# Optimization experiments

Measured on AMD Instinct MI355X. Metric: run time of the kernel, lower is better.

## Reference

```python
import jax, jax.numpy as jnp
import numpy as np

B, L, D, H = 4, 1024, 1024, 16
HD = D // H            # head_dim = 64
MAX_LEN = 1024         # pos_max_len
SCALE = HD ** 0.5


def setup_inputs() -> dict:
    key = jax.random.key(0)
    ks = jax.random.split(key, 7)
    sd = 1.0 / np.sqrt(D)
    x = jax.random.normal(ks[0], (B, L, D), dtype=jnp.float32)
    Wq = jax.random.normal(ks[1], (D, D), dtype=jnp.float32) * sd
    Wk = jax.random.normal(ks[2], (D, D), dtype=jnp.float32) * sd
    Wv = jax.random.normal(ks[3], (D, D), dtype=jnp.float32) * sd
    Wo = jax.random.normal(ks[4], (D, D), dtype=jnp.float32) * sd
    # relative positional embedding tables [2*max_len+1, head_dim]
    pek = jax.random.normal(ks[5], (2 * MAX_LEN + 1, HD), dtype=jnp.float32) / np.sqrt(HD)
    pev = jax.random.normal(ks[6], (2 * MAX_LEN + 1, HD), dtype=jnp.float32) / np.sqrt(HD)
    return {"x": x, "Wq": Wq, "Wk": Wk, "Wv": Wv, "Wo": Wo, "pek": pek, "pev": pev}


def _rel_idx(seq_len):
    r = jnp.arange(seq_len)
    dist = r[None, :] - r[:, None]                 # k - q, [L, L]
    return jnp.clip(dist, -MAX_LEN, MAX_LEN) + MAX_LEN


def reference(x, Wq, Wk, Wv, Wo, pek, pev):
    b, s, _ = x.shape
    # projections (nn.Linear: x @ W.T), split heads -> [b, h, s, d]
    def proj(W):
        return (x @ W.T).reshape(b, s, H, HD).transpose(0, 2, 1, 3)
    Q, K, V = proj(Wq), proj(Wk), proj(Wv)

    scores = jnp.einsum('bhqd,bhkd->bhqk', Q, K) / SCALE
    idx = _rel_idx(s)                              # [s, s]
    rel_k = pek[idx]                               # [s, s, hd]
    scores = scores + jnp.einsum('bhqd,qkd->bhqk', Q, rel_k) / SCALE

    causal = jnp.tril(jnp.ones((s, s), dtype=bool))
    scores = jnp.where(causal[None, None], scores, -jnp.inf)
    attn = jax.nn.softmax(scores, axis=-1)         # [b, h, q, k]

    out = jnp.einsum('bhqk,bhkd->bhqd', attn, V)
    rel_v = pev[idx]                               # [s, s, hd]
    out = out + jnp.einsum('bhqk,qkd->bhqd', attn, rel_v)

    out = out.transpose(0, 2, 1, 3).reshape(b, s, D)
    return out @ Wo.T
```

## Files before the change

### kernel.cpp

```cpp
#include <hip/hip_runtime.h>
#include <hip/hip_bf16.h>

typedef __hip_bfloat16 bf16;
using bfv8 = __attribute__((ext_vector_type(8))) __bf16;
using f4_t = __attribute__((ext_vector_type(4))) float;

#define DEVI static __device__ __forceinline__

DEVI unsigned short f2bu(float f) {
    bf16 h = __float2bfloat16(f);
    return __builtin_bit_cast(unsigned short, h);
}
DEVI ushort4 f4_to_b4(float4 v) {
    ushort4 r;
    r.x = f2bu(v.x); r.y = f2bu(v.y); r.z = f2bu(v.z); r.w = f2bu(v.w);
    return r;
}
DEVI void gl2lds16(const void* g, void* l) {
    __builtin_amdgcn_global_load_lds((const __attribute__((address_space(1))) void*)g,
                                     (__attribute__((address_space(3))) void*)l, 16, 0, 0);
}

template<int N>
DEVI float row_ror(float x) {
    return __builtin_bit_cast(float,
        __builtin_amdgcn_update_dpp(0, __builtin_bit_cast(int, x), 0x120 | N, 0xF, 0xF, false));
}
DEVI float max16(float x) {
    x = fmaxf(x, row_ror<8>(x));
    x = fmaxf(x, row_ror<4>(x));
    x = fmaxf(x, row_ror<2>(x));
    x = fmaxf(x, row_ror<1>(x));
    return x;
}
DEVI float sum16(float x) {
    x += row_ror<8>(x);
    x += row_ror<4>(x);
    x += row_ror<2>(x);
    x += row_ror<1>(x);
    return x;
}

__global__ __launch_bounds__(256) void prep_cast(
    const float* __restrict__ x, const float* __restrict__ wq, const float* __restrict__ wk,
    const float* __restrict__ wv, const float* __restrict__ wo,
    bf16* __restrict__ xb, bf16* __restrict__ wqb, bf16* __restrict__ wkb,
    bf16* __restrict__ wvb, bf16* __restrict__ wob)
{
    size_t i = (size_t)blockIdx.x * 256 + threadIdx.x;
    const size_t X4 = 1u << 20, W4 = 1u << 18;
    const float* src; bf16* dst; size_t off;
    if (i < X4)              { src = x;  dst = xb;  off = i; }
    else if (i < X4 + W4)    { src = wq; dst = wqb; off = i - X4; }
    else if (i < X4 + 2*W4)  { src = wk; dst = wkb; off = i - X4 - W4; }
    else if (i < X4 + 3*W4)  { src = wv; dst = wvb; off = i - X4 - 2*W4; }
    else                     { src = wo; dst = wob; off = i - X4 - 3*W4; }
    float4 v = ((const float4*)src)[off];
    ((ushort4*)dst)[off] = f4_to_b4(v);
}

__global__ __launch_bounds__(256) void prep_blocks(
    const float* __restrict__ pek, const float* __restrict__ pev,
    bf16* __restrict__ pekBlk, bf16* __restrict__ pevBlk)
{
    __shared__ bf16 t[64][72];
    const int b = blockIdx.x;
    const int r = threadIdx.x >> 2, c0 = (threadIdx.x & 3) * 16;

    if (b < 17) {
        const float* src = pek + (size_t)(64 * b + 1 + r) * 64 + c0;
        bf16* dst = pekBlk + (size_t)b * 4096 + r * 64 + c0;
#pragma unroll
        for (int j = 0; j < 16; j += 4)
            *(ushort4*)(dst + j) = f4_to_b4(*(const float4*)(src + j));
    }
    {
        const float* src = pev + (size_t)(64 * b + 1 + r) * 64 + c0;
#pragma unroll
        for (int j = 0; j < 16; j++) t[r][c0 + j] = __float2bfloat16(src[j]);
        __syncthreads();
        bf16* dst = pevBlk + (size_t)b * 4096 + r * 64 + c0;
#pragma unroll
        for (int j = 0; j < 16; j++) dst[j] = t[c0 + j][r];
    }
}

__global__ __launch_bounds__(256, 4) void gemm_bt3(
    const bf16* __restrict__ A,
    const bf16* __restrict__ B0, const bf16* __restrict__ B1, const bf16* __restrict__ B2,
    bf16* __restrict__ outb, bf16* __restrict__ vtb, float* __restrict__ outf,
    int K, int mode)
{
    __shared__ __align__(16) bf16 smem[64 * 64 + 128 * 64];
    bf16* As = smem;
    bf16* Bs = smem + 64 * 64;
    bf16* Cb = smem;

    const int tid  = threadIdx.x;
    const int lane = tid & 63, wave = tid >> 6;
    const int quad = lane >> 4, l16 = lane & 15;
    const int wr = wave >> 1, wc = wave & 1;
    const int m0 = blockIdx.y * 64, n0 = blockIdx.x * 128;
    const int z = blockIdx.z;
    const bf16* Bm = (z == 0) ? B0 : (z == 1) ? B1 : B2;

    f4_t zero = {0.f, 0.f, 0.f, 0.f};
    f4_t acc[2][4];
#pragma unroll
    for (int i = 0; i < 2; i++)
#pragma unroll
        for (int j = 0; j < 4; j++) acc[i][j] = zero;

    const int srow8 = lane >> 3;
    const int scol  = (lane & 7) * 8;
    const bf16* Ag = A  + (size_t)(m0 + 16 * wave + srow8) * K + scol;
    const bf16* Bg = Bm + (size_t)(n0 + 32 * wave + srow8) * K + scol;

    for (int k0 = 0; k0 < K; k0 += 64) {
#pragma unroll
        for (int i = 0; i < 2; i++)
            gl2lds16(Ag + (size_t)(8 * i) * K + k0, &As[(16 * wave + 8 * i) * 64]);
#pragma unroll
        for (int i = 0; i < 4; i++)
            gl2lds16(Bg + (size_t)(8 * i) * K + k0, &Bs[(32 * wave + 8 * i) * 64]);
        __syncthreads();
#pragma unroll
        for (int ks = 0; ks < 2; ks++) {
            bfv8 af[2], bfr[4];
#pragma unroll
            for (int mt = 0; mt < 2; mt++)
                af[mt] = *(const bfv8*)&As[(wr * 32 + mt * 16 + l16) * 64 + ks * 32 + quad * 8];
#pragma unroll
            for (int nt = 0; nt < 4; nt++)
                bfr[nt] = *(const bfv8*)&Bs[(wc * 64 + nt * 16 + l16) * 64 + ks * 32 + quad * 8];
#pragma unroll
            for (int mt = 0; mt < 2; mt++)
#pragma unroll
                for (int nt = 0; nt < 4; nt++)
                    acc[mt][nt] = __builtin_amdgcn_mfma_f32_16x16x32_bf16(af[mt], bfr[nt], acc[mt][nt], 0, 0, 0);
        }
        __syncthreads();
    }

    if (mode == 1) {
#pragma unroll
        for (int mt = 0; mt < 2; mt++)
#pragma unroll
            for (int nt = 0; nt < 4; nt++)
#pragma unroll
                for (int r = 0; r < 4; r++) {
                    int m = m0 + wr * 32 + mt * 16 + quad * 4 + r;
                    int n = n0 + wc * 64 + nt * 16 + l16;
                    outf[(size_t)m * 1024 + n] = acc[mt][nt][r];
                }
        return;
    }

    const int b  = m0 >> 10, l0 = m0 & 1023, h0 = n0 >> 6;
    if (z < 2) {
#pragma unroll
        for (int mt = 0; mt < 2; mt++)
#pragma unroll
            for (int nt = 0; nt < 4; nt++)
#pragma unroll
                for (int r = 0; r < 4; r++) {
                    int mm = wr * 32 + mt * 16 + quad * 4 + r;
                    int nn = wc * 64 + nt * 16 + l16;
                    Cb[mm * 136 + nn] = __float2bfloat16(acc[mt][nt][r]);
                }
        __syncthreads();
        bf16* ob = outb + (size_t)z * (4 * 16 * 1024 * 64);
        const int ri = tid >> 1, hp = ri >> 6, lrow = ri & 63, c0 = (tid & 1) * 32;
        bf16* dst = ob + ((size_t)((b * 16 + h0 + hp) * 1024) + l0 + lrow) * 64 + c0;
        const bf16* srcl = &Cb[lrow * 136 + hp * 64 + c0];
#pragma unroll
        for (int j = 0; j < 4; j++)
            *(int4*)(dst + 8 * j) = *(const int4*)(srcl + 8 * j);
    } else {
#pragma unroll
        for (int mt = 0; mt < 2; mt++)
#pragma unroll
            for (int nt = 0; nt < 4; nt++)
#pragma unroll
                for (int r = 0; r < 4; r++) {
                    int mm = wr * 32 + mt * 16 + quad * 4 + r;
                    int nn = wc * 64 + nt * 16 + l16;
                    Cb[nn * 72 + mm] = __float2bfloat16(acc[mt][nt][r]);
                }
        __syncthreads();
        const int ri = tid >> 1, c0 = (tid & 1) * 32;
        const int n = n0 + ri, h = n >> 6, hd = n & 63;
        bf16* dst = vtb + ((size_t)((b * 16 + h) * 64 + hd)) * 1024 + l0 + c0;
        const bf16* srcl = &Cb[ri * 72 + c0];
#pragma unroll
        for (int j = 0; j < 4; j++)
            *(int4*)(dst + 8 * j) = *(const int4*)(srcl + 8 * j);
    }
}

__global__ __launch_bounds__(256) void attn_k(
    const bf16* __restrict__ Qb, const bf16* __restrict__ Kb, const bf16* __restrict__ Vtb,
    const bf16* __restrict__ pekBlk, const bf16* __restrict__ pevBlk, bf16* __restrict__ Ob)
{
    constexpr int ST = 104;
    __shared__ __align__(16) bf16 Ks[64 * 64];
    __shared__ __align__(16) bf16 Vs[64 * 64];
    __shared__ __align__(16) bf16 pekR[2 * 4096];
    __shared__ __align__(16) bf16 pevR[3 * 4096];
    __shared__ __align__(16) bf16 sU[4][16 * ST];
    __shared__ __align__(16) bf16 sP[4][16 * 72];

    const int tid  = threadIdx.x;
    const int lane = tid & 63, wave = tid >> 6;
    const int quad = lane >> 4, l16 = lane & 15;
    const int bh = blockIdx.x;
    const int g  = 15 - blockIdx.y;
    const int s  = 4 * g + wave;
    const int nkt = g + 1;

    bf16* myU = sU[wave];
    bf16* myP = sP[wave];

    const int srow8 = lane >> 3;
    const int scg   = (lane & 7) ^ srow8;
    const int x8    = l16 & 7;

    {
        int* p = (int*)myU;
#pragma unroll
        for (int i = 0; i < 13; i++) p[lane + 64 * i] = 0;
    }

    bfv8 qf[2];
    {
        const bf16* qp = Qb + ((size_t)bh * 1024 + 16 * s + l16) * 64 + quad * 8;
        qf[0] = *(const bfv8*)qp;
        qf[1] = *(const bfv8*)(qp + 32);
#pragma unroll
        for (int j = 0; j < 8; j++) {
            qf[0][j] = (__bf16)((float)qf[0][j] * 0.125f);
            qf[1][j] = (__bf16)((float)qf[1][j] * 0.125f);
        }
    }

    f4_t zero = {0.f, 0.f, 0.f, 0.f};
    f4_t o_acc[4];
    float m_i[4], l_i[4];
#pragma unroll
    for (int i = 0; i < 4; i++) { o_acc[i] = zero; m_i[i] = -1e30f; l_i[i] = 0.f; }

    const bf16* Kbh = Kb  + (size_t)bh * 1024 * 64;
    const bf16* Vbh = Vtb + (size_t)bh * 64 * 1024;
    const int B0 = 15 - g;

#pragma unroll
    for (int i = 0; i < 2; i++) {
        const int row = 8 * wave + 32 * i + srow8;
        gl2lds16(Kbh + (size_t)row * 64 + scg * 8, &Ks[(8 * wave + 32 * i) * 64]);
        gl2lds16(Vbh + (size_t)row * 1024 + scg * 8, &Vs[(8 * wave + 32 * i) * 64]);
    }
#pragma unroll
    for (int i2 = 0; i2 < 2; i2++) {
        const int slot = (B0 + i2) & 1;
#pragma unroll
        for (int i = 0; i < 2; i++) {
            const int row = 16 * wave + 8 * i + srow8;
            gl2lds16(pekBlk + (size_t)(B0 + i2) * 4096 + row * 64 + scg * 8,
                     &pekR[slot * 4096 + (16 * wave + 8 * i) * 64]);
        }
    }
#pragma unroll
    for (int i2 = 0; i2 < 3; i2++) {
        const int slot = (B0 + i2) % 3;
#pragma unroll
        for (int i = 0; i < 2; i++) {
            const int row = 16 * wave + 8 * i + srow8;
            gl2lds16(pevBlk + (size_t)(B0 + i2) * 4096 + row * 64 + scg * 8,
                     &pevR[slot * 4096 + (16 * wave + 8 * i) * 64]);
        }
    }

    for (int kt = 0; kt < nkt; kt++) {
        const int k0 = kt << 6;
        const int Bb = kt - g + 15;
        const int bm3 = Bb % 3;

        if (kt > 0) {
#pragma unroll
            for (int i = 0; i < 2; i++) {
                const int row = 8 * wave + 32 * i + srow8;
                gl2lds16(Kbh + (size_t)(k0 + row) * 64 + scg * 8, &Ks[(8 * wave + 32 * i) * 64]);
                gl2lds16(Vbh + (size_t)row * 1024 + k0 + scg * 8, &Vs[(8 * wave + 32 * i) * 64]);
            }
            const int bNew = Bb + 1, cNew = Bb + 2;
            const int slotK = bNew & 1, slotV = cNew % 3;
#pragma unroll
            for (int i = 0; i < 2; i++) {
                const int row = 16 * wave + 8 * i + srow8;
                gl2lds16(pekBlk + (size_t)bNew * 4096 + row * 64 + scg * 8,
                         &pekR[slotK * 4096 + (16 * wave + 8 * i) * 64]);
                gl2lds16(pevBlk + (size_t)cNew * 4096 + row * 64 + scg * 8,
                         &pevR[slotV * 4096 + (16 * wave + 8 * i) * 64]);
            }
        }
        __syncthreads();

        f4_t s1[4], tt[5];
#pragma unroll
        for (int i = 0; i < 4; i++) s1[i] = zero;
#pragma unroll
        for (int i = 0; i < 5; i++) tt[i] = zero;
#pragma unroll
        for (int ks = 0; ks < 2; ks++) {
#pragma unroll
            for (int nt = 0; nt < 4; nt++) {
                bfv8 kf = *(const bfv8*)&Ks[(nt * 16 + l16) * 64 + ((ks * 4 + quad) ^ x8) * 8];
                s1[nt] = __builtin_amdgcn_mfma_f32_16x16x32_bf16(qf[ks], kf, s1[nt], 0, 0, 0);
            }
#pragma unroll
            for (int nt = 0; nt < 5; nt++) {
                const int off  = 48 - 16 * wave + 16 * nt;
                const int slot = (Bb + (off >> 6)) & 1;
                bfv8 pf = *(const bfv8*)&pekR[slot * 4096 + ((off & 63) + l16) * 64
                                              + ((ks * 4 + quad) ^ x8) * 8];
                tt[nt] = __builtin_amdgcn_mfma_f32_16x16x32_bf16(qf[ks], pf, tt[nt], 0, 0, 0);
            }
        }

        float sc[4][4];
#pragma unroll
        for (int r = 0; r < 4; r++) {
            int qq = quad * 4 + r;
            int t  = l16 + 15 - qq;
            int srcl = quad * 16 + (t & 15);
            bool lo = (t < 16);
            float rot[5];
#pragma unroll
            for (int j = 0; j < 5; j++) rot[j] = __shfl(tt[j][r], srcl, 64);
#pragma unroll
            for (int nt = 0; nt < 4; nt++) {
                float s2 = lo ? rot[nt] : rot[nt + 1];
                float v = s1[nt][r] + s2;
                int kk = nt * 16 + l16;
                if (k0 + kk > 16 * s + qq) v = -1e30f;
                sc[nt][r] = v;
            }
        }

        float alpha[4];
#pragma unroll
        for (int r = 0; r < 4; r++) {
            float mt = fmaxf(fmaxf(sc[0][r], sc[1][r]), fmaxf(sc[2][r], sc[3][r]));
            mt = max16(mt);
            float mnew = fmaxf(m_i[r], mt);
            alpha[r] = __expf(m_i[r] - mnew);
            m_i[r] = mnew;
        }
#pragma unroll
        for (int nt = 0; nt < 4; nt++)
#pragma unroll
            for (int r = 0; r < 4; r++)
                sc[nt][r] = __expf(sc[nt][r] - m_i[r]);
#pragma unroll
        for (int r = 0; r < 4; r++) {
            float rs = sum16(sc[0][r] + sc[1][r] + sc[2][r] + sc[3][r]);
            l_i[r] = l_i[r] * alpha[r] + rs;
#pragma unroll
            for (int nt = 0; nt < 4; nt++) o_acc[nt][r] *= alpha[r];
        }

#pragma unroll
        for (int nt = 0; nt < 4; nt++)
#pragma unroll
            for (int r = 0; r < 4; r++) {
                int qq = quad * 4 + r;
                int kk = nt * 16 + l16;
                bf16 pb = __float2bfloat16(sc[nt][r]);
                myP[qq * 72 + kk] = pb;
                myU[qq * ST + kk - qq + 15] = pb;
            }

#pragma unroll
        for (int ks = 0; ks < 2; ks++) {
            bfv8 pa = *(const bfv8*)&myP[l16 * 72 + ks * 32 + quad * 8];
#pragma unroll
            for (int nt = 0; nt < 4; nt++) {
                bfv8 vf = *(const bfv8*)&Vs[(nt * 16 + l16) * 64 + ((ks * 4 + quad) ^ x8) * 8];
                o_acc[nt] = __builtin_amdgcn_mfma_f32_16x16x32_bf16(pa, vf, o_acc[nt], 0, 0, 0);
            }
        }
#pragma unroll
        for (int ks = 0; ks < 3; ks++) {
            bfv8 ua = *(const bfv8*)&myU[l16 * ST + ks * 32 + quad * 8];
            const int off2 = 48 - 16 * wave + 32 * ks + 8 * quad;
            int slot2 = bm3 + (off2 >> 6);
            if (slot2 >= 3) slot2 -= 3;
            const int chunk = (((off2 & 63) >> 3) ^ x8);
#pragma unroll
            for (int nt = 0; nt < 4; nt++) {
                bfv8 pvf = *(const bfv8*)&pevR[slot2 * 4096 + (nt * 16 + l16) * 64 + chunk * 8];
                o_acc[nt] = __builtin_amdgcn_mfma_f32_16x16x32_bf16(ua, pvf, o_acc[nt], 0, 0, 0);
            }
        }
        __syncthreads();
    }

    const int b = bh >> 4, h = bh & 15;
#pragma unroll
    for (int nt = 0; nt < 4; nt++)
#pragma unroll
        for (int r = 0; r < 4; r++) {
            int q = 16 * s + quad * 4 + r;
            int d = nt * 16 + l16;
            Ob[((size_t)(b * 1024 + q)) * 1024 + h * 64 + d] = __float2bfloat16(o_acc[nt][r] / l_i[r]);
        }
}

extern "C" void kernel_launch(void* const* d_in, const int* in_sizes, int n_in,
                              void* d_out, int out_size, void* d_ws, size_t ws_size,
                              hipStream_t stream) {
    const float* x   = (const float*)d_in[0];
    const float* Wq  = (const float*)d_in[1];
    const float* Wk  = (const float*)d_in[2];
    const float* Wv  = (const float*)d_in[3];
    const float* Wo  = (const float*)d_in[4];
    const float* pek = (const float*)d_in[5];
    const float* pev = (const float*)d_in[6];

    const size_t MB = 1u << 20;
    char* ws = (char*)d_ws;
    bf16* xb     = (bf16*)(ws + 0);
    bf16* Wqb    = (bf16*)(ws + 8  * MB);
    bf16* Wkb    = (bf16*)(ws + 10 * MB);
    bf16* Wvb    = (bf16*)(ws + 12 * MB);
    bf16* Wob    = (bf16*)(ws + 14 * MB);
    bf16* Qb     = (bf16*)(ws + 16 * MB);
    bf16* Kb     = (bf16*)(ws + 24 * MB);
    bf16* Vtb    = (bf16*)(ws + 32 * MB);
    bf16* pekBlk = (bf16*)(ws + 48 * MB);
    bf16* pevBlk = (bf16*)(ws + 48 * MB + 256*1024);
    bf16* Ao     = xb;

    prep_cast<<<dim3(8192), 256, 0, stream>>>(x, Wq, Wk, Wv, Wo, xb, Wqb, Wkb, Wvb, Wob);
    prep_blocks<<<dim3(18), 256, 0, stream>>>(pek, pev, pekBlk, pevBlk);
    gemm_bt3<<<dim3(8, 64, 3), 256, 0, stream>>>(xb, Wqb, Wkb, Wvb, Qb, Vtb, nullptr, 1024, 0);
    attn_k<<<dim3(64, 16), 256, 0, stream>>>(Qb, Kb, Vtb, pekBlk, pevBlk, Ao);
    gemm_bt3<<<dim3(8, 64, 1), 256, 0, stream>>>(Ao, Wob, nullptr, nullptr, nullptr, nullptr, (float*)d_out, 1024, 1);
}
```

Before: 236.7 us.

## Read relative-position tables directly from global memory instead of staging in LDS

Drops the LDS ring buffers for the pek and pev relative-position blocks along with their async global-to-LDS prefetch. MFMA operands are now loaded directly from global memory through L1/L2, and a launch-bounds occupancy hint of 4 blocks is added. This frees 40KB of LDS per block so more blocks can be resident, at the cost of per-wave global loads on the critical path with more latency and possibly more redundant traffic.

```diff
diff --git a/kernel.cpp b/kernel.cpp
--- a/kernel.cpp
+++ b/kernel.cpp
@@ -198,15 +198,13 @@
     }
 }
 
-__global__ __launch_bounds__(256) void attn_k(
+__global__ __launch_bounds__(256, 4) void attn_k(
     const bf16* __restrict__ Qb, const bf16* __restrict__ Kb, const bf16* __restrict__ Vtb,
     const bf16* __restrict__ pekBlk, const bf16* __restrict__ pevBlk, bf16* __restrict__ Ob)
 {
     constexpr int ST = 104;
     __shared__ __align__(16) bf16 Ks[64 * 64];
     __shared__ __align__(16) bf16 Vs[64 * 64];
-    __shared__ __align__(16) bf16 pekR[2 * 4096];
-    __shared__ __align__(16) bf16 pevR[3 * 4096];
     __shared__ __align__(16) bf16 sU[4][16 * ST];
     __shared__ __align__(16) bf16 sP[4][16 * 72];
 
@@ -251,7 +249,6 @@
 
     const bf16* Kbh = Kb  + (size_t)bh * 1024 * 64;
     const bf16* Vbh = Vtb + (size_t)bh * 64 * 1024;
-    const int B0 = 15 - g;
 
 #pragma unroll
     for (int i = 0; i < 2; i++) {
@@ -259,31 +256,10 @@
         gl2lds16(Kbh + (size_t)row * 64 + scg * 8, &Ks[(8 * wave + 32 * i) * 64]);
         gl2lds16(Vbh + (size_t)row * 1024 + scg * 8, &Vs[(8 * wave + 32 * i) * 64]);
     }
-#pragma unroll
-    for (int i2 = 0; i2 < 2; i2++) {
-        const int slot = (B0 + i2) & 1;
-#pragma unroll
-        for (int i = 0; i < 2; i++) {
-            const int row = 16 * wave + 8 * i + srow8;
-            gl2lds16(pekBlk + (size_t)(B0 + i2) * 4096 + row * 64 + scg * 8,
-                     &pekR[slot * 4096 + (16 * wave + 8 * i) * 64]);
-        }
-    }
-#pragma unroll
-    for (int i2 = 0; i2 < 3; i2++) {
-        const int slot = (B0 + i2) % 3;
-#pragma unroll
-        for (int i = 0; i < 2; i++) {
-            const int row = 16 * wave + 8 * i + srow8;
-            gl2lds16(pevBlk + (size_t)(B0 + i2) * 4096 + row * 64 + scg * 8,
-                     &pevR[slot * 4096 + (16 * wave + 8 * i) * 64]);
-        }
-    }
 
     for (int kt = 0; kt < nkt; kt++) {
         const int k0 = kt << 6;
         const int Bb = kt - g + 15;
-        const int bm3 = Bb % 3;
 
         if (kt > 0) {
 #pragma unroll
@@ -292,16 +268,6 @@
                 gl2lds16(Kbh + (size_t)(k0 + row) * 64 + scg * 8, &Ks[(8 * wave + 32 * i) * 64]);
                 gl2lds16(Vbh + (size_t)row * 1024 + k0 + scg * 8, &Vs[(8 * wave + 32 * i) * 64]);
             }
-            const int bNew = Bb + 1, cNew = Bb + 2;
-            const int slotK = bNew & 1, slotV = cNew % 3;
-#pragma unroll
-            for (int i = 0; i < 2; i++) {
-                const int row = 16 * wave + 8 * i + srow8;
-                gl2lds16(pekBlk + (size_t)bNew * 4096 + row * 64 + scg * 8,
-                         &pekR[slotK * 4096 + (16 * wave + 8 * i) * 64]);
-                gl2lds16(pevBlk + (size_t)cNew * 4096 + row * 64 + scg * 8,
-                         &pevR[slotV * 4096 + (16 * wave + 8 * i) * 64]);
-            }
         }
         __syncthreads();
 
@@ -310,6 +276,7 @@
         for (int i = 0; i < 4; i++) s1[i] = zero;
 #pragma unroll
         for (int i = 0; i < 5; i++) tt[i] = zero;
+        const bf16* pekW = pekBlk + (size_t)(Bb * 64 + 48 - 16 * wave + l16) * 64 + quad * 8;
 #pragma unroll
         for (int ks = 0; ks < 2; ks++) {
 #pragma unroll
@@ -319,10 +286,7 @@
             }
 #pragma unroll
             for (int nt = 0; nt < 5; nt++) {
-                const int off  = 48 - 16 * wave + 16 * nt;
-                const int slot = (Bb + (off >> 6)) & 1;
-                bfv8 pf = *(const bfv8*)&pekR[slot * 4096 + ((off & 63) + l16) * 64
-                                              + ((ks * 4 + quad) ^ x8) * 8];
+                bfv8 pf = *(const bfv8*)(pekW + (size_t)(nt * 16) * 64 + ks * 32);
                 tt[nt] = __builtin_amdgcn_mfma_f32_16x16x32_bf16(qf[ks], pf, tt[nt], 0, 0, 0);
             }
         }
@@ -392,13 +356,11 @@
 #pragma unroll
         for (int ks = 0; ks < 3; ks++) {
             bfv8 ua = *(const bfv8*)&myU[l16 * ST + ks * 32 + quad * 8];
-            const int off2 = 48 - 16 * wave + 32 * ks + 8 * quad;
-            int slot2 = bm3 + (off2 >> 6);
-            if (slot2 >= 3) slot2 -= 3;
-            const int chunk = (((off2 & 63) >> 3) ^ x8);
+            const int t0 = Bb * 64 + 48 - 16 * wave + 32 * ks + 8 * quad;
+            const bf16* pvW = pevBlk + (size_t)(t0 >> 6) * 4096 + (t0 & 63);
 #pragma unroll
             for (int nt = 0; nt < 4; nt++) {
-                bfv8 pvf = *(const bfv8*)&pevR[slot2 * 4096 + (nt * 16 + l16) * 64 + chunk * 8];
+                bfv8 pvf = *(const bfv8*)(pvW + (size_t)(nt * 16 + l16) * 64);
                 o_acc[nt] = __builtin_amdgcn_mfma_f32_16x16x32_bf16(ua, pvf, o_acc[nt], 0, 0, 0);
             }
         }
```

New measurement: 298.4 us. 26.1% more time.

## Prefetch next K/V and rel-pos tiles into registers during compute

Applied to the files above, without the earlier changes.

Replaces direct global-to-LDS loads issued at the top of each iteration with register-staged prefetch of the next tile's K, V, pek and pev blocks. The loads are issued before the current tile's MFMA work and written to LDS after a barrier, so global latency is meant to hide behind compute. It also sets launch_bounds min blocks to 2 to cap register use. The cost is extra VGPRs for staging and an added barrier per iteration, with possible spills under the tighter register limit.

```diff
diff --git a/kernel.cpp b/kernel.cpp
--- a/kernel.cpp
+++ b/kernel.cpp
@@ -198,7 +198,7 @@
     }
 }
 
-__global__ __launch_bounds__(256) void attn_k(
+__global__ __launch_bounds__(256, 2) void attn_k(
     const bf16* __restrict__ Qb, const bf16* __restrict__ Kb, const bf16* __restrict__ Vtb,
     const bf16* __restrict__ pekBlk, const bf16* __restrict__ pevBlk, bf16* __restrict__ Ob)
 {
@@ -279,31 +279,32 @@
                      &pevR[slot * 4096 + (16 * wave + 8 * i) * 64]);
         }
     }
+    __syncthreads();
+
+    bfv8 stK[2], stV[2], stPk[2], stPv[2];
 
     for (int kt = 0; kt < nkt; kt++) {
         const int k0 = kt << 6;
         const int Bb = kt - g + 15;
         const int bm3 = Bb % 3;
-
-        if (kt > 0) {
+        const bool pf = (kt + 1 < nkt);
+
+        if (pf) {
+            const int k0n = (kt + 1) << 6;
+            const int bNew = Bb + 2, cNew = Bb + 3;
 #pragma unroll
             for (int i = 0; i < 2; i++) {
                 const int row = 8 * wave + 32 * i + srow8;
-                gl2lds16(Kbh + (size_t)(k0 + row) * 64 + scg * 8, &Ks[(8 * wave + 32 * i) * 64]);
-                gl2lds16(Vbh + (size_t)row * 1024 + k0 + scg * 8, &Vs[(8 * wave + 32 * i) * 64]);
-            }
-            const int bNew = Bb + 1, cNew = Bb + 2;
-            const int slotK = bNew & 1, slotV = cNew % 3;
+                stK[i] = *(const bfv8*)(Kbh + (size_t)(k0n + row) * 64 + scg * 8);
+                stV[i] = *(const bfv8*)(Vbh + (size_t)row * 1024 + k0n + scg * 8);
+            }
 #pragma unroll
             for (int i = 0; i < 2; i++) {
                 const int row = 16 * wave + 8 * i + srow8;
-                gl2lds16(pekBlk + (size_t)bNew * 4096 + row * 64 + scg * 8,
-                         &pekR[slotK * 4096 + (16 * wave + 8 * i) * 64]);
-                gl2lds16(pevBlk + (size_t)cNew * 4096 + row * 64 + scg * 8,
-                         &pevR[slotV * 4096 + (16 * wave + 8 * i) * 64]);
-            }
-        }
-        __syncthreads();
+                stPk[i] = *(const bfv8*)(pekBlk + (size_t)bNew * 4096 + row * 64 + scg * 8);
+                stPv[i] = *(const bfv8*)(pevBlk + (size_t)cNew * 4096 + row * 64 + scg * 8);
+            }
+        }
 
         f4_t s1[4], tt[5];
 #pragma unroll
@@ -321,9 +322,9 @@
             for (int nt = 0; nt < 5; nt++) {
                 const int off  = 48 - 16 * wave + 16 * nt;
                 const int slot = (Bb + (off >> 6)) & 1;
-                bfv8 pf = *(const bfv8*)&pekR[slot * 4096 + ((off & 63) + l16) * 64
+                bfv8 pfr = *(const bfv8*)&pekR[slot * 4096 + ((off & 63) + l16) * 64
                                               + ((ks * 4 + quad) ^ x8) * 8];
-                tt[nt] = __builtin_amdgcn_mfma_f32_16x16x32_bf16(qf[ks], pf, tt[nt], 0, 0, 0);
+                tt[nt] = __builtin_amdgcn_mfma_f32_16x16x32_bf16(qf[ks], pfr, tt[nt], 0, 0, 0);
             }
         }
 
@@ -400,6 +401,22 @@
             for (int nt = 0; nt < 4; nt++) {
                 bfv8 pvf = *(const bfv8*)&pevR[slot2 * 4096 + (nt * 16 + l16) * 64 + chunk * 8];
                 o_acc[nt] = __builtin_amdgcn_mfma_f32_16x16x32_bf16(ua, pvf, o_acc[nt], 0, 0, 0);
+            }
+        }
+        __syncthreads();
+
+        if (pf) {
+            const int Bn = Bb + 1;
+            const int slotK = (Bn + 1) & 1, slotV = (Bn + 2) % 3;
+#pragma unroll
+            for (int i = 0; i < 2; i++) {
+                *(bfv8*)&Ks[(8 * wave + 32 * i) * 64 + lane * 8] = stK[i];
+                *(bfv8*)&Vs[(8 * wave + 32 * i) * 64 + lane * 8] = stV[i];
+            }
+#pragma unroll
+            for (int i = 0; i < 2; i++) {
+                *(bfv8*)&pekR[slotK * 4096 + (16 * wave + 8 * i) * 64 + lane * 8] = stPk[i];
+                *(bfv8*)&pevR[slotV * 4096 + (16 * wave + 8 * i) * 64 + lane * 8] = stPv[i];
             }
         }
         __syncthreads();
```

Result: faster. 225.8 us (-4.6%).
